# Kernel optimization log

Measured on AMD Instinct MI355X. Metric: run time of the kernel, lower is better.

## Reference

```python
import jax, jax.numpy as jnp
import numpy as np

NUM_GRAPHS = 512
EPS = 1e-5

def squash(x):
    # capsule squash: (|x|^2 / (1 + |x|^2)) * x / |x|
    n2 = jnp.sum(x * x, axis=-1, keepdims=True)
    return (n2 / (1.0 + n2)) * x * jax.lax.rsqrt(n2 + 1e-12)

def setup_inputs():
    key = jax.random.key(0)
    ks = jax.random.split(key, 16)
    N, E, F, H, L, C = 100000, 600000, 128, 128, 3, 2
    x = jax.random.normal(ks[0], (N, F), jnp.float32)
    edge_index = jax.random.randint(ks[1], (2, E), 0, N)
    batch = jnp.sort(jax.random.randint(ks[2], (N,), 0, NUM_GRAPHS))
    def lin(k, i, o):
        return (jax.random.normal(k, (i, o), jnp.float32) / np.sqrt(i)).astype(jnp.float32)
    return {
        'x': x, 'edge_index': edge_index, 'batch': batch,
        'bn_gamma': jnp.ones((F,), jnp.float32), 'bn_beta': jnp.zeros((F,), jnp.float32),
        'W0': lin(ks[3], F, H), 'b0': jnp.zeros((H,), jnp.float32),
        'W1': lin(ks[4], H, H), 'b1': jnp.zeros((H,), jnp.float32),
        'W2': lin(ks[5], H, H), 'b2': jnp.zeros((H,), jnp.float32),
        'tar_w': (jax.random.normal(ks[6], (L, H), jnp.float32) / np.sqrt(H)).astype(jnp.float32),
        'lin1_w': lin(ks[7], 3 * H, H), 'lin1_b': jnp.zeros((H,), jnp.float32),
        'lin2_w': lin(ks[8], H, C), 'lin2_b': jnp.zeros((C,), jnp.float32),
    }

def reference(x, edge_index, batch, bn_gamma, bn_beta, W0, b0, W1, b1, W2, b2,
              tar_w, lin1_w, lin1_b, lin2_w, lin2_b):
    N, G = x.shape[0], NUM_GRAPHS
    # input BatchNorm1d (training-mode batch statistics)
    mu = jnp.mean(x, 0)
    var = jnp.var(x, 0)
    h = (x - mu) * jax.lax.rsqrt(var + EPS) * bn_gamma + bn_beta
    # remove_self_loops + add_remaining_self_loops ~= append diagonal with weight 1
    loops = jnp.arange(N)
    src = jnp.concatenate([edge_index[0], loops])
    dst = jnp.concatenate([edge_index[1], loops])
    w = jnp.ones((src.shape[0],), h.dtype)
    # GCN symmetric normalization D^-1/2 A D^-1/2
    deg = jax.ops.segment_sum(w, dst, num_segments=N)
    dinv = jax.lax.rsqrt(jnp.maximum(deg, 1e-12))
    norm = dinv[src] * w * dinv[dst]  # [E+N]
    ones_n = jnp.ones((N,), h.dtype)
    cnt = jax.ops.segment_sum(ones_n, batch, num_segments=G)  # nodes per graph
    cnt_safe = jnp.maximum(cnt, 1.0)[:, None]
    graph_rep = jnp.zeros((G, 3 * W0.shape[1]), h.dtype)
    loss_stability = jnp.zeros((), h.dtype)
    for i, (W, b) in enumerate([(W0, b0), (W1, b1), (W2, b2)]):
        m = h @ W  # [N, H]
        agg = jax.ops.segment_sum(norm[:, None] * m[src], dst, num_segments=N) + b
        h = squash(agg)
        loss_stability = loss_stability + jnp.mean((agg - h) ** 2)
        # Task-Aware Readout: node attention then fused sum / mean / max scatters
        attn = h @ tar_w[i]  # [N]
        x_wsum = jax.ops.segment_sum(attn[:, None] * h, batch, num_segments=G)
        x_mean = jax.ops.segment_sum(h, batch, num_segments=G) / cnt_safe
        x_max = jax.ops.segment_max(h, batch, num_segments=G)
        x_max = jnp.where(cnt[:, None] > 0, x_max, 0.0)
        graph_rep = graph_rep + jnp.concatenate([x_wsum, x_mean, x_max], axis=-1)
    z = jax.nn.relu(graph_rep @ lin1_w + lin1_b)
    z = z @ lin2_w + lin2_b
    return jax.nn.log_softmax(z, axis=-1)
```

## Files before the change

### kernel.cpp

```cpp
#include <hip/hip_runtime.h>
#include <hip/hip_bf16.h>
#include <math.h>

#define BN_EPS 1e-5f
#define BN_BLOCKS 512
#define NCHUNK 256

typedef __attribute__((ext_vector_type(8)))  short short8v;
typedef __attribute__((ext_vector_type(16))) float f32x16;

__device__ __forceinline__ unsigned short f2bf(float f){
  union { float f; unsigned u; } v; v.f = f;
  unsigned r = v.u + 0x7FFFu + ((v.u >> 16) & 1u);
  return (unsigned short)(r >> 16);
}
__device__ __forceinline__ float bf2f(unsigned short b){
  union { unsigned u; float f; } v; v.u = ((unsigned)b) << 16;
  return v.f;
}
__device__ __forceinline__ float2 bfpair(unsigned u){
  union { unsigned u; float f; } lo, hi;
  lo.u = u << 16;
  hi.u = u & 0xFFFF0000u;
  return make_float2(lo.f, hi.f);
}
__device__ __forceinline__ unsigned packbf(float a, float b){
  return (unsigned)f2bf(a) | ((unsigned)f2bf(b) << 16);
}

__global__ __launch_bounds__(256) void bn_part(const float* __restrict__ x,
                                               float* __restrict__ part, int total4){
  const float4* x4 = (const float4*)x;
  int stride = gridDim.x * blockDim.x;
  float4 s = make_float4(0.f,0.f,0.f,0.f);
  float4 q = make_float4(0.f,0.f,0.f,0.f);
  for (int idx = blockIdx.x*blockDim.x + threadIdx.x; idx < total4; idx += stride){
    float4 v = x4[idx];
    s.x += v.x; s.y += v.y; s.z += v.z; s.w += v.w;
    q.x += v.x*v.x; q.y += v.y*v.y; q.z += v.z*v.z; q.w += v.w*v.w;
  }
  __shared__ float4 shs[256], shq[256];
  shs[threadIdx.x] = s; shq[threadIdx.x] = q;
  __syncthreads();
  if (threadIdx.x < 32){
    int c4 = threadIdx.x;
    float4 ts = shs[c4], tq = shq[c4];
    #pragma unroll
    for (int j = 1; j < 8; ++j){
      float4 os = shs[c4 + j*32], oq = shq[c4 + j*32];
      ts.x += os.x; ts.y += os.y; ts.z += os.z; ts.w += os.w;
      tq.x += oq.x; tq.y += oq.y; tq.z += oq.z; tq.w += oq.w;
    }
    float* pb = part + (size_t)blockIdx.x * 256;
    *(float4*)(pb + c4*4)       = ts;
    *(float4*)(pb + 128 + c4*4) = tq;
  }
}

__global__ __launch_bounds__(256) void bn_reduce(const float* __restrict__ part,
                                                 const float* __restrict__ gamma,
                                                 const float* __restrict__ beta,
                                                 float* __restrict__ scale,
                                                 float* __restrict__ shift, int N){
  int t = threadIdx.x;
  float a0=0.f,a1=0.f,a2=0.f,a3=0.f,a4=0.f,a5=0.f,a6=0.f,a7=0.f;
  for (int b = 0; b < BN_BLOCKS; b += 8){
    a0 += part[(size_t)(b+0)*256 + t];
    a1 += part[(size_t)(b+1)*256 + t];
    a2 += part[(size_t)(b+2)*256 + t];
    a3 += part[(size_t)(b+3)*256 + t];
    a4 += part[(size_t)(b+4)*256 + t];
    a5 += part[(size_t)(b+5)*256 + t];
    a6 += part[(size_t)(b+6)*256 + t];
    a7 += part[(size_t)(b+7)*256 + t];
  }
  float acc = ((a0+a1)+(a2+a3)) + ((a4+a5)+(a6+a7));
  __shared__ float sh[256];
  sh[t] = acc;
  __syncthreads();
  if (t < 128){
    float mu  = sh[t] / (float)N;
    float var = sh[t+128] / (float)N - mu*mu;
    float sc  = gamma[t] * rsqrtf(var + BN_EPS);
    scale[t] = sc;
    shift[t] = beta[t] - mu*sc;
  }
}


__global__ __launch_bounds__(256) void chunk_hist(const int* __restrict__ dst,
                                                  int* __restrict__ hist2,
                                                  int E, int NB, int CH){
  __shared__ int lh[512];
  for (int i = threadIdx.x; i < NB; i += 256) lh[i] = 0;
  __syncthreads();
  int c = blockIdx.x;
  int e0 = c*CH, e1 = min(e0 + CH, E);
  for (int e = e0 + threadIdx.x; e < e1; e += 256)
    atomicAdd(&lh[dst[e] >> 8], 1);
  __syncthreads();
  for (int i = threadIdx.x; i < NB; i += 256)
    hist2[c*NB + i] = lh[i];
}

__global__ __launch_bounds__(512) void chunk_scan(const int* __restrict__ hist2,
                                                  int* __restrict__ offs2,
                                                  int* __restrict__ bbase,
                                                  int NB, int E){
  __shared__ int tot[512];
  int b = threadIdx.x;
  int total = 0;
  if (b < NB){
    for (int c = 0; c < NCHUNK; c += 8){
      int h0 = hist2[(c+0)*NB + b], h1 = hist2[(c+1)*NB + b];
      int h2 = hist2[(c+2)*NB + b], h3 = hist2[(c+3)*NB + b];
      int h4 = hist2[(c+4)*NB + b], h5 = hist2[(c+5)*NB + b];
      int h6 = hist2[(c+6)*NB + b], h7 = hist2[(c+7)*NB + b];
      total += ((h0+h1)+(h2+h3)) + ((h4+h5)+(h6+h7));
    }
  }
  tot[b] = (b < NB) ? total : 0;
  __syncthreads();
  int v = tot[b];
  for (int d = 1; d < 512; d <<= 1){
    int u = (b >= d) ? tot[b-d] : 0;
    __syncthreads();
    tot[b] += u;
    __syncthreads();
  }
  if (b < NB){
    int base = tot[b] - v;
    bbase[b] = base;
    int run = base;
    for (int c = 0; c < NCHUNK; c += 8){
      int h0 = hist2[(c+0)*NB + b], h1 = hist2[(c+1)*NB + b];
      int h2 = hist2[(c+2)*NB + b], h3 = hist2[(c+3)*NB + b];
      int h4 = hist2[(c+4)*NB + b], h5 = hist2[(c+5)*NB + b];
      int h6 = hist2[(c+6)*NB + b], h7 = hist2[(c+7)*NB + b];
      offs2[(c+0)*NB + b] = run; run += h0;
      offs2[(c+1)*NB + b] = run; run += h1;
      offs2[(c+2)*NB + b] = run; run += h2;
      offs2[(c+3)*NB + b] = run; run += h3;
      offs2[(c+4)*NB + b] = run; run += h4;
      offs2[(c+5)*NB + b] = run; run += h5;
      offs2[(c+6)*NB + b] = run; run += h6;
      offs2[(c+7)*NB + b] = run; run += h7;
    }
  }
  if (b == 0) bbase[NB] = E;
}

__global__ __launch_bounds__(256) void chunk_scatter(const int* __restrict__ src,
                                                     const int* __restrict__ dst,
                                                     const int* __restrict__ offs2,
                                                     unsigned* __restrict__ ebuf,
                                                     int E, int NB, int CH){
  __shared__ int lcur[512];
  int c = blockIdx.x;
  for (int i = threadIdx.x; i < NB; i += 256) lcur[i] = offs2[c*NB + i];
  __syncthreads();
  int e0 = c*CH, e1 = min(e0 + CH, E);
  for (int e = e0 + threadIdx.x; e < e1; e += 256){
    int d = dst[e];
    int b = d >> 8;
    int pos = atomicAdd(&lcur[b], 1);
    ebuf[pos] = ((unsigned)(d & 255) << 24) | (unsigned)src[e];
  }
}

__global__ __launch_bounds__(256) void bucket_sort(const unsigned* __restrict__ ebuf,
                                                   const int* __restrict__ bbase,
                                                   int* __restrict__ csrs,
                                                   int* __restrict__ rowstart,
                                                   float* __restrict__ dinv,
                                                   int N, int E, int NB){
  int b = blockIdx.x;
  int base = bbase[b];
  int end  = bbase[b+1];
  int len  = end - base;
  int tid = threadIdx.x;
  __shared__ int cnt[256];
  __shared__ int pref[256];
  cnt[tid] = 0;
  __syncthreads();
  for (int i = tid; i < len; i += 256)
    atomicAdd(&cnt[ebuf[base + i] >> 24], 1);
  __syncthreads();
  int v = cnt[tid];
  pref[tid] = v;
  __syncthreads();
  for (int d = 1; d < 256; d <<= 1){
    int u = (tid >= d) ? pref[tid-d] : 0;
    __syncthreads();
    pref[tid] += u;
    __syncthreads();
  }
  int excl = pref[tid] - v;
  int node = b*256 + tid;
  if (node < N){
    rowstart[node] = base + excl;
    dinv[node] = rsqrtf((float)v + 1.0f);
  }
  cnt[tid] = excl;
  __syncthreads();
  for (int i = tid; i < len; i += 256){
    unsigned r = ebuf[base + i];
    int pos = atomicAdd(&cnt[r >> 24], 1);
    csrs[base + pos] = (int)(r & 0xFFFFFFu);
  }
  if (b == NB-1 && tid == 0) rowstart[N] = E;
}

__global__ void gbounds(const int* __restrict__ batch, int* __restrict__ gstart, int N, int G){
  int g = blockIdx.x*blockDim.x + threadIdx.x;
  if (g > G) return;
  int lo = 0, hi = N;
  while (lo < hi){ int mid = (lo+hi)>>1; if (batch[mid] < g) lo = mid+1; else hi = mid; }
  gstart[g] = lo;
}

__global__ void prep_w(const float* __restrict__ W0, const float* __restrict__ W1,
                       const float* __restrict__ W2, const float* __restrict__ scale,
                       unsigned short* __restrict__ Wh){
  int idx = blockIdx.x*blockDim.x + threadIdx.x;
  if (idx >= 3*16384) return;
  int l = idx >> 14, r = idx & 16383, c = r >> 7, k = r & 127;
  const float* W = (l==0) ? W0 : (l==1) ? W1 : W2;
  float v = W[k*128 + c];
  if (l == 0) v *= scale[k];
  Wh[idx] = f2bf(v);
}

__global__ __launch_bounds__(128) void prep_bias0(const float* __restrict__ b0,
                                                  const float* __restrict__ shift,
                                                  const float* __restrict__ W0,
                                                  float* __restrict__ bias0p){
  int j = threadIdx.x;
  __shared__ float sh[128];
  sh[j] = shift[j];
  __syncthreads();
  float s = b0[j];
  for (int c = 0; c < 128; ++c) s += sh[c] * W0[c*128 + j];
  bias0p[j] = s;
}

template<int CVT>
__global__ __launch_bounds__(512) void gemm_mfma(
    const float* __restrict__ A32, const unsigned short* __restrict__ A16,
    const unsigned short* __restrict__ Bh, unsigned short* __restrict__ C, int N){
  __shared__ unsigned short Ah[64*128];
  int tid = threadIdx.x;
  int r0 = blockIdx.x * 64;
  int w = tid >> 6, lane = tid & 63;
  int rt = w & 1;
  int ct = (w >> 1) * 32;
  int lrow = 32*rt + (lane & 31);
  int khalf = lane >> 5;
  int c0 = ct + (lane & 31);
  const unsigned short* bh0 = Bh + (size_t)c0*128 + khalf*8;

  short8v bhf[8];
  #pragma unroll
  for (int s = 0; s < 8; ++s) bhf[s] = *(const short8v*)(bh0 + s*16);

  if (CVT){
    #pragma unroll
    for (int it = 0; it < 4; ++it){
      int idx = tid + it*512;
      int row = idx >> 5;
      int c4  = idx & 31;
      int r = r0 + row;
      float4 av = (r < N) ? *(const float4*)(A32 + (size_t)r*128 + c4*4)
                          : make_float4(0.f,0.f,0.f,0.f);
      int byte0 = (c4*8) ^ ((row & 15) << 4);
      uint2 p = make_uint2(packbf(av.x, av.y), packbf(av.z, av.w));
      *(uint2*)((char*)Ah + row*256 + byte0) = p;
    }
  } else {
    #pragma unroll
    for (int it = 0; it < 2; ++it){
      int idx = tid + it*512;
      int row = idx >> 4;
      int c8  = idx & 15;
      int r = r0 + row;
      uint4 v = (r < N) ? *(const uint4*)(A16 + (size_t)r*128 + c8*8)
                        : make_uint4(0,0,0,0);
      int byte0 = (c8*16) ^ ((row & 15) << 4);
      *(uint4*)((char*)Ah + row*256 + byte0) = v;
    }
  }
  __syncthreads();

  f32x16 acc = {};
  const char* AhB = (const char*)Ah + lrow*256;
  int sw = (lrow & 15) << 4;
  #pragma unroll
  for (int s = 0; s < 8; ++s){
    int abyte = (s*32 + khalf*16) ^ sw;
    short8v a = *(const short8v*)(AhB + abyte);
    acc = __builtin_amdgcn_mfma_f32_32x32x16_bf16(a, bhf[s], acc, 0, 0, 0);
  }

  #pragma unroll
  for (int r = 0; r < 16; ++r){
    int row = r0 + 32*rt + (r & 3) + 8*(r >> 2) + 4*khalf;
    if (row < N) C[(size_t)row*128 + c0] = f2bf(acc[r]);
  }
}

__global__ __launch_bounds__(256) void gather_squash(
    const unsigned short* __restrict__ m, const int* __restrict__ rowstart,
    const int* __restrict__ csrs, const float* __restrict__ dinv,
    const float* __restrict__ bias, const float* __restrict__ tar,
    unsigned short* __restrict__ h, float* __restrict__ attn, int N){
  int node = blockIdx.x*8 + (threadIdx.x >> 5);
  if (node >= N) return;
  int lane = threadIdx.x & 31;
  const uint2* m2 = (const uint2*)m;
  float dv = dinv[node];
  float sn = dv*dv;
  uint2 sv = m2[(size_t)node*32 + lane];
  float2 p0 = bfpair(sv.x), p1 = bfpair(sv.y);
  float a0 = p0.x*sn, a1 = p0.y*sn, a2 = p1.x*sn, a3 = p1.y*sn;
  int j0 = rowstart[node], j1 = rowstart[node+1];

  for (int base = j0; base < j1; base += 32){
    int cnt = j1 - base; if (cnt > 32) cnt = 32;
    int sidx = 0; float swt = 0.f;
    if (lane < cnt){
      sidx = csrs[base + lane];
      swt  = dinv[sidx] * dv;
    }
    int t = 0;
    for (; t + 4 <= cnt; t += 4){
      int s0 = __shfl(sidx, t, 32),   s1 = __shfl(sidx, t+1, 32);
      int s2 = __shfl(sidx, t+2, 32), s3 = __shfl(sidx, t+3, 32);
      float w0 = __shfl(swt, t, 32),   w1 = __shfl(swt, t+1, 32);
      float w2 = __shfl(swt, t+2, 32), w3 = __shfl(swt, t+3, 32);
      uint2 u0 = m2[(size_t)s0*32 + lane];
      uint2 u1 = m2[(size_t)s1*32 + lane];
      uint2 u2 = m2[(size_t)s2*32 + lane];
      uint2 u3 = m2[(size_t)s3*32 + lane];
      float2 q0, q1;
      q0 = bfpair(u0.x); q1 = bfpair(u0.y);
      a0 += w0*q0.x; a1 += w0*q0.y; a2 += w0*q1.x; a3 += w0*q1.y;
      q0 = bfpair(u1.x); q1 = bfpair(u1.y);
      a0 += w1*q0.x; a1 += w1*q0.y; a2 += w1*q1.x; a3 += w1*q1.y;
      q0 = bfpair(u2.x); q1 = bfpair(u2.y);
      a0 += w2*q0.x; a1 += w2*q0.y; a2 += w2*q1.x; a3 += w2*q1.y;
      q0 = bfpair(u3.x); q1 = bfpair(u3.y);
      a0 += w3*q0.x; a1 += w3*q0.y; a2 += w3*q1.x; a3 += w3*q1.y;
    }
    if (cnt - t >= 2){
      int s0 = __shfl(sidx, t, 32), s1 = __shfl(sidx, t+1, 32);
      float w0 = __shfl(swt, t, 32), w1 = __shfl(swt, t+1, 32);
      uint2 u0 = m2[(size_t)s0*32 + lane];
      uint2 u1 = m2[(size_t)s1*32 + lane];
      float2 q0 = bfpair(u0.x), q1 = bfpair(u0.y);
      a0 += w0*q0.x; a1 += w0*q0.y; a2 += w0*q1.x; a3 += w0*q1.y;
      q0 = bfpair(u1.x); q1 = bfpair(u1.y);
      a0 += w1*q0.x; a1 += w1*q0.y; a2 += w1*q1.x; a3 += w1*q1.y;
      t += 2;
    }
    if (t < cnt){
      int s0 = __shfl(sidx, t, 32);
      float w0 = __shfl(swt, t, 32);
      uint2 u0 = m2[(size_t)s0*32 + lane];
      float2 q0 = bfpair(u0.x), q1 = bfpair(u0.y);
      a0 += w0*q0.x; a1 += w0*q0.y; a2 += w0*q1.x; a3 += w0*q1.y;
    }
  }

  float4 bv = ((const float4*)bias)[lane];
  a0 += bv.x; a1 += bv.y; a2 += bv.z; a3 += bv.w;
  float n2 = a0*a0 + a1*a1 + a2*a2 + a3*a3;
  #pragma unroll
  for (int o = 16; o > 0; o >>= 1) n2 += __shfl_xor(n2, o);
  float sc = (n2/(1.f+n2)) * rsqrtf(n2 + 1e-12f);
  float h0 = a0*sc, h1 = a1*sc, h2 = a2*sc, h3 = a3*sc;
  ((uint2*)(h + (size_t)node*128))[lane] = make_uint2(packbf(h0,h1), packbf(h2,h3));
  float4 tv = ((const float4*)tar)[lane];
  float at = h0*tv.x + h1*tv.y + h2*tv.z + h3*tv.w;
  #pragma unroll
  for (int o = 16; o > 0; o >>= 1) at += __shfl_xor(at, o);
  if (lane == 0) attn[node] = at;
}

__global__ __launch_bounds__(1024) void readout(const unsigned short* __restrict__ h,
                                                const float* __restrict__ attn,
                                                const int* __restrict__ gstart,
                                                float* __restrict__ grep){
  int g = blockIdx.x;
  int t   = threadIdx.x & 63;
  int grp = threadIdx.x >> 6;
  int a = gstart[g], b = gstart[g+1];
  float wsx = 0.f, wsy = 0.f, smx_ = 0.f, smy_ = 0.f;
  float mxx = -INFINITY, mxy = -INFINITY;
  for (int n = a + grp; n < b; n += 16){
    unsigned u = ((const unsigned*)(h + (size_t)n*128))[t];
    float2 v = bfpair(u);
    float at = attn[n];
    wsx += at*v.x; wsy += at*v.y;
    smx_ += v.x;  smy_ += v.y;
    mxx = fmaxf(mxx, v.x); mxy = fmaxf(mxy, v.y);
  }
  __shared__ float2 sws[16][64], ssm[16][64], smx[16][64];
  sws[grp][t] = make_float2(wsx, wsy);
  ssm[grp][t] = make_float2(smx_, smy_);
  smx[grp][t] = make_float2(mxx, mxy);
  __syncthreads();
  if (grp == 0){
    #pragma unroll
    for (int j = 1; j < 16; ++j){
      float2 ow = sws[j][t], os = ssm[j][t], om = smx[j][t];
      wsx += ow.x; wsy += ow.y;
      smx_ += os.x; smy_ += os.y;
      mxx = fmaxf(mxx, om.x); mxy = fmaxf(mxy, om.y);
    }
    int cnt = b - a;
    float inv = 1.f / fmaxf((float)cnt, 1.f);
    if (cnt == 0){ mxx = 0.f; mxy = 0.f; }
    grep[(size_t)g*384 + t*2]           += wsx;
    grep[(size_t)g*384 + t*2 + 1]       += wsy;
    grep[(size_t)g*384 + 128 + t*2]     += smx_*inv;
    grep[(size_t)g*384 + 128 + t*2 + 1] += smy_*inv;
    grep[(size_t)g*384 + 256 + t*2]     += mxx;
    grep[(size_t)g*384 + 256 + t*2 + 1] += mxy;
  }
}

__global__ __launch_bounds__(128) void classify(const float* __restrict__ grep,
                                                const float* __restrict__ w1, const float* __restrict__ b1,
                                                const float* __restrict__ w2, const float* __restrict__ b2,
                                                float* __restrict__ out){
  int g = blockIdx.x, t = threadIdx.x;
  __shared__ float gr[384];
  for (int i = t; i < 384; i += 128) gr[i] = grep[(size_t)g*384 + i];
  __syncthreads();
  float z = b1[t];
  for (int k = 0; k < 384; ++k) z += gr[k]*w1[k*128 + t];
  z = fmaxf(z, 0.f);
  float c0 = z*w2[t*2 + 0], c1 = z*w2[t*2 + 1];
  #pragma unroll
  for (int o = 32; o > 0; o >>= 1){ c0 += __shfl_xor(c0, o); c1 += __shfl_xor(c1, o); }
  __shared__ float r0s[2], r1s[2];
  if ((t & 63) == 0){ r0s[t>>6] = c0; r1s[t>>6] = c1; }
  __syncthreads();
  if (t == 0){
    float z0 = r0s[0] + r0s[1] + b2[0];
    float z1 = r1s[0] + r1s[1] + b2[1];
    float mm = fmaxf(z0, z1);
    float lse = mm + logf(expf(z0-mm) + expf(z1-mm));
    out[g*2 + 0] = z0 - lse;
    out[g*2 + 1] = z1 - lse;
  }
}

extern "C" void kernel_launch(void* const* d_in, const int* in_sizes, int n_in,
                              void* d_out, int out_size, void* d_ws, size_t ws_size,
                              hipStream_t stream) {
  const float* x     = (const float*)d_in[0];
  const int*   ei    = (const int*)d_in[1];
  const int*   batch = (const int*)d_in[2];
  const float* gamma = (const float*)d_in[3];
  const float* beta  = (const float*)d_in[4];
  const float* W0    = (const float*)d_in[5];
  const float* b0    = (const float*)d_in[6];
  const float* W1    = (const float*)d_in[7];
  const float* b1    = (const float*)d_in[8];
  const float* W2    = (const float*)d_in[9];
  const float* b2    = (const float*)d_in[10];
  const float* tar   = (const float*)d_in[11];
  const float* l1w   = (const float*)d_in[12];
  const float* l1b   = (const float*)d_in[13];
  const float* l2w   = (const float*)d_in[14];
  const float* l2b   = (const float*)d_in[15];
  float* out = (float*)d_out;

  int N = in_sizes[0] / 128;
  int E = in_sizes[1] / 2;
  int G = out_size / 2;
  const int* srcp = ei;
  const int* dstp = ei + E;

  char* wsb = (char*)d_ws;
  size_t off = 0;
  auto alloc = [&](size_t bytes)->char*{
    char* p = wsb + off; off += (bytes + 255) & ~(size_t)255; return p;
  };
  unsigned short* h = (unsigned short*)alloc((size_t)N*128*2);
  unsigned short* m = (unsigned short*)alloc((size_t)N*128*2);
  float* attn    = (float*)alloc((size_t)N*4);
  float* dinv    = (float*)alloc((size_t)N*4);
  int*   rowst   = (int*)  alloc((size_t)(N+1)*4);
  int*   csrs    = (int*)  alloc((size_t)E*4);
  unsigned* ebuf = (unsigned*)alloc((size_t)E*4);
  int*   hist2   = (int*)  alloc((size_t)NCHUNK*512*4);
  int*   offs2   = (int*)  alloc((size_t)NCHUNK*512*4);
  int*   bbase   = (int*)  alloc(513*4);
  int*   gstart  = (int*)  alloc((size_t)(G+1)*4);
  float* grep    = (float*)alloc((size_t)G*384*4);
  float* stats   = (float*)alloc(2*128*4);
  float* bias0p  = (float*)alloc(128*4);
  float* part    = (float*)alloc((size_t)BN_BLOCKS*256*4);
  unsigned short* Wh = (unsigned short*)alloc(3*16384*2);
  (void)ws_size;

  float* scale  = stats;
  float* shift  = stats + 128;

  int NB = (N + 255) >> 8;
  int CH = (E + NCHUNK - 1) / NCHUNK;
  hipMemsetAsync(grep, 0, (size_t)G*384*4, stream);

  chunk_hist<<<NCHUNK, 256, 0, stream>>>(dstp, hist2, E, NB, CH);
  chunk_scan<<<1, 512, 0, stream>>>(hist2, offs2, bbase, NB, E);
  chunk_scatter<<<NCHUNK, 256, 0, stream>>>(srcp, dstp, offs2, ebuf, E, NB, CH);
  bucket_sort<<<NB, 256, 0, stream>>>(ebuf, bbase, csrs, rowst, dinv, N, E, NB);
  gbounds<<<(G+1+255)/256, 256, 0, stream>>>(batch, gstart, N, G);

  bn_part<<<BN_BLOCKS, 256, 0, stream>>>(x, part, N*32);
  bn_reduce<<<1, 256, 0, stream>>>(part, gamma, beta, scale, shift, N);
  prep_w<<<(3*16384+255)/256, 256, 0, stream>>>(W0, W1, W2, scale, Wh);
  prep_bias0<<<1, 128, 0, stream>>>(b0, shift, W0, bias0p);

  const float* bs[3] = {bias0p, b1, b2};
  int nb64 = (N + 63) / 64;
  for (int l = 0; l < 3; ++l){
    if (l == 0)
      gemm_mfma<1><<<nb64, 512, 0, stream>>>(x, nullptr, Wh, m, N);
    else
      gemm_mfma<0><<<nb64, 512, 0, stream>>>(nullptr, h, Wh + l*16384, m, N);
    gather_squash<<<(N+7)/8, 256, 0, stream>>>(m, rowst, csrs, dinv, bs[l], tar + l*128, h, attn, N);
    readout<<<G, 1024, 0, stream>>>(h, attn, gstart, grep);
  }
  classify<<<G, 128, 0, stream>>>(grep, l1w, l1b, l2w, l2b, out);
}
```

Before: 277.5 us.

## Merge independent preprocessing kernels into fewer multi-role launches

Combines the edge histogram with BatchNorm partial sums, the chunk scan with the BN reduce and graph-boundary search, and the bucket sort with weight/bias preparation into single launches that branch on block index. The aim is to cut the number of small serialized kernel launches and let independent work share the GPU at the same time. This adds branch-heavy kernels whose shared-memory footprint is the union of all roles, which may reduce occupancy. The offs2 loop is also simplified to a non-unrolled form.

```diff
diff --git a/kernel.cpp b/kernel.cpp
--- a/kernel.cpp
+++ b/kernel.cpp
@@ -3,7 +3,6 @@
 #include <math.h>
 
 #define BN_EPS 1e-5f
-#define BN_BLOCKS 512
 #define NCHUNK 256
 
 typedef __attribute__((ext_vector_type(8)))  short short8v;
@@ -13,10 +12,6 @@
   union { float f; unsigned u; } v; v.f = f;
   unsigned r = v.u + 0x7FFFu + ((v.u >> 16) & 1u);
   return (unsigned short)(r >> 16);
-}
-__device__ __forceinline__ float bf2f(unsigned short b){
-  union { unsigned u; float f; } v; v.u = ((unsigned)b) << 16;
-  return v.f;
 }
 __device__ __forceinline__ float2 bfpair(unsigned u){
   union { unsigned u; float f; } lo, hi;
@@ -28,126 +23,128 @@
   return (unsigned)f2bf(a) | ((unsigned)f2bf(b) << 16);
 }
 
-__global__ __launch_bounds__(256) void bn_part(const float* __restrict__ x,
-                                               float* __restrict__ part, int total4){
-  const float4* x4 = (const float4*)x;
-  int stride = gridDim.x * blockDim.x;
-  float4 s = make_float4(0.f,0.f,0.f,0.f);
-  float4 q = make_float4(0.f,0.f,0.f,0.f);
-  for (int idx = blockIdx.x*blockDim.x + threadIdx.x; idx < total4; idx += stride){
-    float4 v = x4[idx];
-    s.x += v.x; s.y += v.y; s.z += v.z; s.w += v.w;
-    q.x += v.x*v.x; q.y += v.y*v.y; q.z += v.z*v.z; q.w += v.w*v.w;
-  }
-  __shared__ float4 shs[256], shq[256];
-  shs[threadIdx.x] = s; shq[threadIdx.x] = q;
-  __syncthreads();
-  if (threadIdx.x < 32){
-    int c4 = threadIdx.x;
-    float4 ts = shs[c4], tq = shq[c4];
-    #pragma unroll
-    for (int j = 1; j < 8; ++j){
-      float4 os = shs[c4 + j*32], oq = shq[c4 + j*32];
-      ts.x += os.x; ts.y += os.y; ts.z += os.z; ts.w += os.w;
-      tq.x += oq.x; tq.y += oq.y; tq.z += oq.z; tq.w += oq.w;
-    }
-    float* pb = part + (size_t)blockIdx.x * 256;
-    *(float4*)(pb + c4*4)       = ts;
-    *(float4*)(pb + 128 + c4*4) = tq;
-  }
-}
-
-__global__ __launch_bounds__(256) void bn_reduce(const float* __restrict__ part,
-                                                 const float* __restrict__ gamma,
-                                                 const float* __restrict__ beta,
-                                                 float* __restrict__ scale,
-                                                 float* __restrict__ shift, int N){
+__global__ __launch_bounds__(256) void k_hist_bn(const int* __restrict__ dst,
+                                                 int* __restrict__ hist2, int E, int NB, int CH,
+                                                 const float* __restrict__ x,
+                                                 float* __restrict__ part, int total4){
+  int tid = threadIdx.x;
+  if (blockIdx.x < NCHUNK){
+    __shared__ int lh[512];
+    for (int i = tid; i < NB; i += 256) lh[i] = 0;
+    __syncthreads();
+    int c = blockIdx.x;
+    int e0 = c*CH, e1 = min(e0 + CH, E);
+    for (int e = e0 + tid; e < e1; e += 256)
+      atomicAdd(&lh[dst[e] >> 8], 1);
+    __syncthreads();
+    for (int i = tid; i < NB; i += 256)
+      hist2[c*NB + i] = lh[i];
+  } else {
+    const float4* x4 = (const float4*)x;
+    int bb = blockIdx.x - NCHUNK;
+    int stride = 512 * 256;
+    float4 s = make_float4(0.f,0.f,0.f,0.f);
+    float4 q = make_float4(0.f,0.f,0.f,0.f);
+    for (int idx = bb*256 + tid; idx < total4; idx += stride){
+      float4 v = x4[idx];
+      s.x += v.x; s.y += v.y; s.z += v.z; s.w += v.w;
+      q.x += v.x*v.x; q.y += v.y*v.y; q.z += v.z*v.z; q.w += v.w*v.w;
+    }
+    __shared__ float4 shs[256], shq[256];
+    shs[tid] = s; shq[tid] = q;
+    __syncthreads();
+    if (tid < 32){
+      int c4 = tid;
+      float4 ts = shs[c4], tq = shq[c4];
+      #pragma unroll
+      for (int j = 1; j < 8; ++j){
+        float4 os = shs[c4 + j*32], oq = shq[c4 + j*32];
+        ts.x += os.x; ts.y += os.y; ts.z += os.z; ts.w += os.w;
+        tq.x += oq.x; tq.y += oq.y; tq.z += oq.z; tq.w += oq.w;
+      }
+      float* pb = part + (size_t)bb * 256;
+      *(float4*)(pb + c4*4)       = ts;
+      *(float4*)(pb + 128 + c4*4) = tq;
+    }
+  }
+}
+
+__global__ __launch_bounds__(512) void k_scan_red_gb(const int* __restrict__ hist2,
+                                                     int* __restrict__ offs2,
+                                                     int* __restrict__ bbase, int NB, int E,
+                                                     const float* __restrict__ part,
+                                                     const float* __restrict__ gamma,
+                                                     const float* __restrict__ beta,
+                                                     float* __restrict__ scale,
+                                                     float* __restrict__ shift, int N,
+                                                     const int* __restrict__ batch,
+                                                     int* __restrict__ gstart, int G){
   int t = threadIdx.x;
-  float a0=0.f,a1=0.f,a2=0.f,a3=0.f,a4=0.f,a5=0.f,a6=0.f,a7=0.f;
-  for (int b = 0; b < BN_BLOCKS; b += 8){
-    a0 += part[(size_t)(b+0)*256 + t];
-    a1 += part[(size_t)(b+1)*256 + t];
-    a2 += part[(size_t)(b+2)*256 + t];
-    a3 += part[(size_t)(b+3)*256 + t];
-    a4 += part[(size_t)(b+4)*256 + t];
-    a5 += part[(size_t)(b+5)*256 + t];
-    a6 += part[(size_t)(b+6)*256 + t];
-    a7 += part[(size_t)(b+7)*256 + t];
-  }
-  float acc = ((a0+a1)+(a2+a3)) + ((a4+a5)+(a6+a7));
-  __shared__ float sh[256];
-  sh[t] = acc;
-  __syncthreads();
-  if (t < 128){
-    float mu  = sh[t] / (float)N;
-    float var = sh[t+128] / (float)N - mu*mu;
-    float sc  = gamma[t] * rsqrtf(var + BN_EPS);
-    scale[t] = sc;
-    shift[t] = beta[t] - mu*sc;
-  }
-}
-
-
-__global__ __launch_bounds__(256) void chunk_hist(const int* __restrict__ dst,
-                                                  int* __restrict__ hist2,
-                                                  int E, int NB, int CH){
-  __shared__ int lh[512];
-  for (int i = threadIdx.x; i < NB; i += 256) lh[i] = 0;
-  __syncthreads();
-  int c = blockIdx.x;
-  int e0 = c*CH, e1 = min(e0 + CH, E);
-  for (int e = e0 + threadIdx.x; e < e1; e += 256)
-    atomicAdd(&lh[dst[e] >> 8], 1);
-  __syncthreads();
-  for (int i = threadIdx.x; i < NB; i += 256)
-    hist2[c*NB + i] = lh[i];
-}
-
-__global__ __launch_bounds__(512) void chunk_scan(const int* __restrict__ hist2,
-                                                  int* __restrict__ offs2,
-                                                  int* __restrict__ bbase,
-                                                  int NB, int E){
-  __shared__ int tot[512];
-  int b = threadIdx.x;
-  int total = 0;
-  if (b < NB){
-    for (int c = 0; c < NCHUNK; c += 8){
-      int h0 = hist2[(c+0)*NB + b], h1 = hist2[(c+1)*NB + b];
-      int h2 = hist2[(c+2)*NB + b], h3 = hist2[(c+3)*NB + b];
-      int h4 = hist2[(c+4)*NB + b], h5 = hist2[(c+5)*NB + b];
-      int h6 = hist2[(c+6)*NB + b], h7 = hist2[(c+7)*NB + b];
-      total += ((h0+h1)+(h2+h3)) + ((h4+h5)+(h6+h7));
-    }
-  }
-  tot[b] = (b < NB) ? total : 0;
-  __syncthreads();
-  int v = tot[b];
-  for (int d = 1; d < 512; d <<= 1){
-    int u = (b >= d) ? tot[b-d] : 0;
-    __syncthreads();
-    tot[b] += u;
-    __syncthreads();
-  }
-  if (b < NB){
-    int base = tot[b] - v;
-    bbase[b] = base;
-    int run = base;
-    for (int c = 0; c < NCHUNK; c += 8){
-      int h0 = hist2[(c+0)*NB + b], h1 = hist2[(c+1)*NB + b];
-      int h2 = hist2[(c+2)*NB + b], h3 = hist2[(c+3)*NB + b];
-      int h4 = hist2[(c+4)*NB + b], h5 = hist2[(c+5)*NB + b];
-      int h6 = hist2[(c+6)*NB + b], h7 = hist2[(c+7)*NB + b];
-      offs2[(c+0)*NB + b] = run; run += h0;
-      offs2[(c+1)*NB + b] = run; run += h1;
-      offs2[(c+2)*NB + b] = run; run += h2;
-      offs2[(c+3)*NB + b] = run; run += h3;
-      offs2[(c+4)*NB + b] = run; run += h4;
-      offs2[(c+5)*NB + b] = run; run += h5;
-      offs2[(c+6)*NB + b] = run; run += h6;
-      offs2[(c+7)*NB + b] = run; run += h7;
-    }
-  }
-  if (b == 0) bbase[NB] = E;
+  if (blockIdx.x == 0){
+    __shared__ int tot[512];
+    int b = t;
+    int total = 0;
+    if (b < NB){
+      for (int c = 0; c < NCHUNK; c += 8){
+        int h0 = hist2[(c+0)*NB + b], h1 = hist2[(c+1)*NB + b];
+        int h2 = hist2[(c+2)*NB + b], h3 = hist2[(c+3)*NB + b];
+        int h4 = hist2[(c+4)*NB + b], h5 = hist2[(c+5)*NB + b];
+        int h6 = hist2[(c+6)*NB + b], h7 = hist2[(c+7)*NB + b];
+        total += ((h0+h1)+(h2+h3)) + ((h4+h5)+(h6+h7));
+      }
+    }
+    tot[b] = (b < NB) ? total : 0;
+    __syncthreads();
+    int v = tot[b];
+    for (int d = 1; d < 512; d <<= 1){
+      int u = (b >= d) ? tot[b-d] : 0;
+      __syncthreads();
+      tot[b] += u;
+      __syncthreads();
+    }
+    if (b < NB){
+      int base = tot[b] - v;
+      bbase[b] = base;
+      int run = base;
+      for (int c = 0; c < NCHUNK; ++c){
+        offs2[c*NB + b] = run;
+        run += hist2[c*NB + b];
+      }
+    }
+    if (b == 0) bbase[NB] = E;
+  } else if (blockIdx.x == 1){
+    if (t < 256){
+      float a0=0.f,a1=0.f,a2=0.f,a3=0.f,a4=0.f,a5=0.f,a6=0.f,a7=0.f;
+      for (int b = 0; b < 512; b += 8){
+        a0 += part[(size_t)(b+0)*256 + t];
+        a1 += part[(size_t)(b+1)*256 + t];
+        a2 += part[(size_t)(b+2)*256 + t];
+        a3 += part[(size_t)(b+3)*256 + t];
+        a4 += part[(size_t)(b+4)*256 + t];
+        a5 += part[(size_t)(b+5)*256 + t];
+        a6 += part[(size_t)(b+6)*256 + t];
+        a7 += part[(size_t)(b+7)*256 + t];
+      }
+      float acc = ((a0+a1)+(a2+a3)) + ((a4+a5)+(a6+a7));
+      __shared__ float sh[256];
+      sh[t] = acc;
+      __syncthreads();
+      if (t < 128){
+        float mu  = sh[t] / (float)N;
+        float var = sh[t+128] / (float)N - mu*mu;
+        float sc  = gamma[t] * rsqrtf(var + BN_EPS);
+        scale[t] = sc;
+        shift[t] = beta[t] - mu*sc;
+      }
+    }
+  } else {
+    int g = (blockIdx.x - 2)*512 + t;
+    if (g <= G){
+      int lo = 0, hi = N;
+      while (lo < hi){ int mid = (lo+hi)>>1; if (batch[mid] < g) lo = mid+1; else hi = mid; }
+      gstart[g] = lo;
+    }
+  }
 }
 
 __global__ __launch_bounds__(256) void chunk_scatter(const int* __restrict__ src,
@@ -168,80 +165,73 @@
   }
 }
 
-__global__ __launch_bounds__(256) void bucket_sort(const unsigned* __restrict__ ebuf,
+__global__ __launch_bounds__(256) void k_sort_prep(const unsigned* __restrict__ ebuf,
                                                    const int* __restrict__ bbase,
                                                    int* __restrict__ csrs,
                                                    int* __restrict__ rowstart,
                                                    float* __restrict__ dinv,
-                                                   int N, int E, int NB){
-  int b = blockIdx.x;
-  int base = bbase[b];
-  int end  = bbase[b+1];
-  int len  = end - base;
+                                                   int N, int E, int NB,
+                                                   const float* __restrict__ W0,
+                                                   const float* __restrict__ W1,
+                                                   const float* __restrict__ W2,
+                                                   const float* __restrict__ scale,
+                                                   unsigned short* __restrict__ Wh,
+                                                   const float* __restrict__ b0,
+                                                   const float* __restrict__ shift,
+                                                   float* __restrict__ bias0p){
   int tid = threadIdx.x;
-  __shared__ int cnt[256];
-  __shared__ int pref[256];
-  cnt[tid] = 0;
-  __syncthreads();
-  for (int i = tid; i < len; i += 256)
-    atomicAdd(&cnt[ebuf[base + i] >> 24], 1);
-  __syncthreads();
-  int v = cnt[tid];
-  pref[tid] = v;
-  __syncthreads();
-  for (int d = 1; d < 256; d <<= 1){
-    int u = (tid >= d) ? pref[tid-d] : 0;
-    __syncthreads();
-    pref[tid] += u;
-    __syncthreads();
-  }
-  int excl = pref[tid] - v;
-  int node = b*256 + tid;
-  if (node < N){
-    rowstart[node] = base + excl;
-    dinv[node] = rsqrtf((float)v + 1.0f);
-  }
-  cnt[tid] = excl;
-  __syncthreads();
-  for (int i = tid; i < len; i += 256){
-    unsigned r = ebuf[base + i];
-    int pos = atomicAdd(&cnt[r >> 24], 1);
-    csrs[base + pos] = (int)(r & 0xFFFFFFu);
-  }
-  if (b == NB-1 && tid == 0) rowstart[N] = E;
-}
-
-__global__ void gbounds(const int* __restrict__ batch, int* __restrict__ gstart, int N, int G){
-  int g = blockIdx.x*blockDim.x + threadIdx.x;
-  if (g > G) return;
-  int lo = 0, hi = N;
-  while (lo < hi){ int mid = (lo+hi)>>1; if (batch[mid] < g) lo = mid+1; else hi = mid; }
-  gstart[g] = lo;
-}
-
-__global__ void prep_w(const float* __restrict__ W0, const float* __restrict__ W1,
-                       const float* __restrict__ W2, const float* __restrict__ scale,
-                       unsigned short* __restrict__ Wh){
-  int idx = blockIdx.x*blockDim.x + threadIdx.x;
-  if (idx >= 3*16384) return;
-  int l = idx >> 14, r = idx & 16383, c = r >> 7, k = r & 127;
-  const float* W = (l==0) ? W0 : (l==1) ? W1 : W2;
-  float v = W[k*128 + c];
-  if (l == 0) v *= scale[k];
-  Wh[idx] = f2bf(v);
-}
-
-__global__ __launch_bounds__(128) void prep_bias0(const float* __restrict__ b0,
-                                                  const float* __restrict__ shift,
-                                                  const float* __restrict__ W0,
-                                                  float* __restrict__ bias0p){
-  int j = threadIdx.x;
-  __shared__ float sh[128];
-  sh[j] = shift[j];
-  __syncthreads();
-  float s = b0[j];
-  for (int c = 0; c < 128; ++c) s += sh[c] * W0[c*128 + j];
-  bias0p[j] = s;
+  if ((int)blockIdx.x < NB){
+    int b = blockIdx.x;
+    int base = bbase[b];
+    int end  = bbase[b+1];
+    int len  = end - base;
+    __shared__ int cnt[256];
+    __shared__ int pref[256];
+    cnt[tid] = 0;
+    __syncthreads();
+    for (int i = tid; i < len; i += 256)
+      atomicAdd(&cnt[ebuf[base + i] >> 24], 1);
+    __syncthreads();
+    int v = cnt[tid];
+    pref[tid] = v;
+    __syncthreads();
+    for (int d = 1; d < 256; d <<= 1){
+      int u = (tid >= d) ? pref[tid-d] : 0;
+      __syncthreads();
+      pref[tid] += u;
+      __syncthreads();
+    }
+    int excl = pref[tid] - v;
+    int node = b*256 + tid;
+    if (node < N){
+      rowstart[node] = base + excl;
+      dinv[node] = rsqrtf((float)v + 1.0f);
+    }
+    cnt[tid] = excl;
+    __syncthreads();
+    for (int i = tid; i < len; i += 256){
+      unsigned r = ebuf[base + i];
+      int pos = atomicAdd(&cnt[r >> 24], 1);
+      csrs[base + pos] = (int)(r & 0xFFFFFFu);
+    }
+    if (b == NB-1 && tid == 0) rowstart[N] = E;
+  } else if ((int)blockIdx.x < NB + 192){
+    int idx = (blockIdx.x - NB)*256 + tid;
+    int l = idx >> 14, r = idx & 16383, c = r >> 7, k = r & 127;
+    const float* W = (l==0) ? W0 : (l==1) ? W1 : W2;
+    float v = W[k*128 + c];
+    if (l == 0) v *= scale[k];
+    Wh[idx] = f2bf(v);
+  } else {
+    __shared__ float sh[128];
+    if (tid < 128) sh[tid] = shift[tid];
+    __syncthreads();
+    if (tid < 128){
+      float s = b0[tid];
+      for (int c = 0; c < 128; ++c) s += sh[c] * W0[c*128 + tid];
+      bias0p[tid] = s;
+    }
+  }
 }
 
 template<int CVT>
@@ -502,7 +492,7 @@
   float* grep    = (float*)alloc((size_t)G*384*4);
   float* stats   = (float*)alloc(2*128*4);
   float* bias0p  = (float*)alloc(128*4);
-  float* part    = (float*)alloc((size_t)BN_BLOCKS*256*4);
+  float* part    = (float*)alloc((size_t)512*256*4);
   unsigned short* Wh = (unsigned short*)alloc(3*16384*2);
   (void)ws_size;
 
@@ -513,16 +503,13 @@
   int CH = (E + NCHUNK - 1) / NCHUNK;
   hipMemsetAsync(grep, 0, (size_t)G*384*4, stream);
 
-  chunk_hist<<<NCHUNK, 256, 0, stream>>>(dstp, hist2, E, NB, CH);
-  chunk_scan<<<1, 512, 0, stream>>>(hist2, offs2, bbase, NB, E);
+  k_hist_bn<<<NCHUNK + 512, 256, 0, stream>>>(dstp, hist2, E, NB, CH, x, part, N*32);
+  k_scan_red_gb<<<4, 512, 0, stream>>>(hist2, offs2, bbase, NB, E,
+                                       part, gamma, beta, scale, shift, N,
+                                       batch, gstart, G);
   chunk_scatter<<<NCHUNK, 256, 0, stream>>>(srcp, dstp, offs2, ebuf, E, NB, CH);
-  bucket_sort<<<NB, 256, 0, stream>>>(ebuf, bbase, csrs, rowst, dinv, N, E, NB);
-  gbounds<<<(G+1+255)/256, 256, 0, stream>>>(batch, gstart, N, G);
-
-  bn_part<<<BN_BLOCKS, 256, 0, stream>>>(x, part, N*32);
-  bn_reduce<<<1, 256, 0, stream>>>(part, gamma, beta, scale, shift, N);
-  prep_w<<<(3*16384+255)/256, 256, 0, stream>>>(W0, W1, W2, scale, Wh);
-  prep_bias0<<<1, 128, 0, stream>>>(b0, shift, W0, bias0p);
+  k_sort_prep<<<NB + 193, 256, 0, stream>>>(ebuf, bbase, csrs, rowst, dinv, N, E, NB,
+                                            W0, W1, W2, scale, Wh, b0, shift, bias0p);
 
   const float* bs[3] = {bias0p, b1, b2};
   int nb64 = (N + 63) / 64;
```

New measurement: 252.4 us. -9.1%, faster.
